# Optimization experiments

Measured on AMD Instinct MI355X. Metric: run time of the kernel, lower is better.

The kernel has to match this reference:

```python
import jax, jax.numpy as jnp
import numpy as np

NUM_SCOPES, NUM_DECOMPS, BATCH, NODES_IN, NUM_SUMS = 128, 8, 1024, 32, 32


def logmatmul(a, b):
    """Stable log-domain matmul: out[..., b, j] = logsumexp_k(a[..., b, k] + b[..., k, j]).
    a: [s, d, B, K], b: [s, d, K, J] -> [s, d, B, J]."""
    max_a = jnp.max(a, axis=-1, keepdims=True)            # [s, d, B, 1]
    max_b = jnp.max(b, axis=-2, keepdims=True)            # [s, d, 1, J]
    prod = jnp.einsum('sdbk,sdkj->sdbj', jnp.exp(a - max_a), jnp.exp(b - max_b))
    return jnp.log(prod) + max_a + max_b


def setup_inputs() -> dict:
    key = jax.random.key(0)
    k1, k2 = jax.random.split(key)
    x = jax.random.normal(k1, (NUM_SCOPES, NUM_DECOMPS, BATCH, NODES_IN), dtype=jnp.float32)
    # accumulators are linear-space (logspace_accumulators=False) and must be > 0
    accumulators = jax.random.uniform(
        k2, (NUM_SCOPES, NUM_DECOMPS, NODES_IN, NUM_SUMS),
        minval=0.1, maxval=1.0, dtype=jnp.float32)
    return {"x": x, "accumulators": accumulators}


def reference(x, accumulators):
    # log_softmax over the nodes_in axis (axis=2) of log(accumulators)
    log_weights = jax.nn.log_softmax(jnp.log(accumulators), axis=2)
    return logmatmul(x, log_weights)  # [s, d, B, num_sums]
```

## Files before the change

kernel.cpp:

```cpp
#include <hip/hip_runtime.h>
#include <stdint.h>


#define THREADS 256
#define ROWS    128

typedef __attribute__((ext_vector_type(8))) short short8;
typedef __attribute__((ext_vector_type(4))) float f32x4;
typedef __attribute__((ext_vector_type(4))) int   i32x4;

__device__ __forceinline__ uint32_t pack2_bf16(float lo, float hi) {
    uint32_t ul = __builtin_bit_cast(uint32_t, lo);
    uint32_t uh = __builtin_bit_cast(uint32_t, hi);
    ul = (ul + 0x7fffu + ((ul >> 16) & 1u)) >> 16;
    uh = (uh + 0x7fffu + ((uh >> 16) & 1u)) >> 16;
    return ul | (uh << 16);
}

__device__ __forceinline__ unsigned short bf16_1(float v) {
    uint32_t u = __builtin_bit_cast(uint32_t, v);
    return (unsigned short)((u + 0x7fffu + ((u >> 16) & 1u)) >> 16);
}

__global__ __launch_bounds__(THREADS, 8) void sws_kernel(
    const float* __restrict__ x,
    const float* __restrict__ acc,
    float* __restrict__ out)
{
    __shared__ float w_f32[32 * 32];
    __shared__ float inv_lds[32];
    __shared__ __align__(16) unsigned short wt_lds[32 * 32];

    const int t    = threadIdx.x;
    const int blk  = blockIdx.x;
    const int sd   = blk >> 3;
    const int lane = t & 63;
    const int wv   = t >> 6;
    const int l15  = lane & 15;
    const int quad = lane >> 4;

    const float4* x4 = (const float4*)(x + (size_t)blk * ROWS * 32);
    float4 xv[4];
#pragma unroll
    for (int i = 0; i < 2; ++i) {
        int f4 = ((wv * 2 + i) * 16 + l15) * 8 + quad * 2;
        xv[2 * i]     = x4[f4];
        xv[2 * i + 1] = x4[f4 + 1];
    }

    const float4 a4 = ((const float4*)(acc + (size_t)sd * 1024))[t];
    *((float4*)&w_f32[t * 4]) = a4;
    __syncthreads();
    if (t < 32) {
        float s = 0.f;
#pragma unroll
        for (int k = 0; k < 32; ++k) s += w_f32[k * 32 + t];
        inv_lds[t] = 1.0f / s;
    }
    __syncthreads();
    {
        const int k = t >> 3, j0 = (t & 7) * 4;
        const float4 inv4 = *((const float4*)&inv_lds[j0]);
        wt_lds[(j0 + 0) * 32 + k] = bf16_1(a4.x * inv4.x);
        wt_lds[(j0 + 1) * 32 + k] = bf16_1(a4.y * inv4.y);
        wt_lds[(j0 + 2) * 32 + k] = bf16_1(a4.z * inv4.z);
        wt_lds[(j0 + 3) * 32 + k] = bf16_1(a4.w * inv4.w);
    }

    float  mrow[2];
    short8 afrag[2];
#pragma unroll
    for (int i = 0; i < 2; ++i) {
        float4 a = xv[2 * i], b = xv[2 * i + 1];
        float m = fmaxf(fmaxf(fmaxf(a.x, a.y), fmaxf(a.z, a.w)),
                        fmaxf(fmaxf(b.x, b.y), fmaxf(b.z, b.w)));
        m = fmaxf(m, __shfl_xor(m, 16, 64));
        m = fmaxf(m, __shfl_xor(m, 32, 64));
        mrow[i] = m;
        i32x4 pk;
        pk[0] = (int)pack2_bf16(__expf(a.x - m), __expf(a.y - m));
        pk[1] = (int)pack2_bf16(__expf(a.z - m), __expf(a.w - m));
        pk[2] = (int)pack2_bf16(__expf(b.x - m), __expf(b.y - m));
        pk[3] = (int)pack2_bf16(__expf(b.z - m), __expf(b.w - m));
        afrag[i] = __builtin_bit_cast(short8, pk);
    }
    __syncthreads();

    short8 bfrag[2];
#pragma unroll
    for (int jt = 0; jt < 2; ++jt)
        bfrag[jt] = *(const short8*)&wt_lds[(jt * 16 + l15) * 32 + quad * 8];

    f32x4 cacc[2][2];
#pragma unroll
    for (int i = 0; i < 2; ++i)
#pragma unroll
        for (int jt = 0; jt < 2; ++jt)
            cacc[i][jt] = __builtin_amdgcn_mfma_f32_16x16x32_bf16(
                afrag[i], bfrag[jt], (f32x4){0.f, 0.f, 0.f, 0.f}, 0, 0, 0);

    float* ob = out + (size_t)blk * ROWS * 32;
#pragma unroll
    for (int i = 0; i < 2; ++i) {
        int rbase = ((wv * 2 + i) * 16) + quad * 4;
#pragma unroll
        for (int r = 0; r < 4; ++r) {
            float mr = __shfl(mrow[i], quad * 4 + r, 16);
            float* orow = ob + (size_t)(rbase + r) * 32;
            orow[l15]      = __logf(cacc[i][0][r]) + mr;
            orow[l15 + 16] = __logf(cacc[i][1][r]) + mr;
        }
    }
}

extern "C" void kernel_launch(void* const* d_in, const int* in_sizes, int n_in,
                              void* d_out, int out_size, void* d_ws, size_t ws_size,
                              hipStream_t stream) {
    const float* x   = (const float*)d_in[0];
    const float* acc = (const float*)d_in[1];
    float* out = (float*)d_out;

    dim3 grid(8192);
    dim3 block(THREADS);
    hipLaunchKernelGGL(sws_kernel, grid, block, 0, stream, x, acc, out);
}
```

Measured before the change: 231.1 us.

## Swap MFMA operands for float4 output stores and pad weight LDS pitch

The MFMA operands are swapped so each lane holds four consecutive output columns of a single row. Output can then be written as float4 stores, and the per-row max no longer needs a shuffle. The transposed weight tile in LDS gets a padded pitch of 40 to reduce bank conflicts on the scattered writes and fragment reads. The kernel is bandwidth-bound, so the main aim is fewer, wider global store instructions.

```diff
diff --git a/kernel.cpp b/kernel.cpp
--- a/kernel.cpp
+++ b/kernel.cpp
@@ -4,6 +4,7 @@
 
 #define THREADS 256
 #define ROWS    128
+#define WPITCH  40
 
 typedef __attribute__((ext_vector_type(8))) short short8;
 typedef __attribute__((ext_vector_type(4))) float f32x4;
@@ -29,7 +30,7 @@
 {
     __shared__ float w_f32[32 * 32];
     __shared__ float inv_lds[32];
-    __shared__ __align__(16) unsigned short wt_lds[32 * 32];
+    __shared__ __align__(16) unsigned short wt_lds[32 * WPITCH];
 
     const int t    = threadIdx.x;
     const int blk  = blockIdx.x;
@@ -61,10 +62,10 @@
     {
         const int k = t >> 3, j0 = (t & 7) * 4;
         const float4 inv4 = *((const float4*)&inv_lds[j0]);
-        wt_lds[(j0 + 0) * 32 + k] = bf16_1(a4.x * inv4.x);
-        wt_lds[(j0 + 1) * 32 + k] = bf16_1(a4.y * inv4.y);
-        wt_lds[(j0 + 2) * 32 + k] = bf16_1(a4.z * inv4.z);
-        wt_lds[(j0 + 3) * 32 + k] = bf16_1(a4.w * inv4.w);
+        wt_lds[(j0 + 0) * WPITCH + k] = bf16_1(a4.x * inv4.x);
+        wt_lds[(j0 + 1) * WPITCH + k] = bf16_1(a4.y * inv4.y);
+        wt_lds[(j0 + 2) * WPITCH + k] = bf16_1(a4.z * inv4.z);
+        wt_lds[(j0 + 3) * WPITCH + k] = bf16_1(a4.w * inv4.w);
     }
 
     float  mrow[2];
@@ -89,7 +90,7 @@
     short8 bfrag[2];
 #pragma unroll
     for (int jt = 0; jt < 2; ++jt)
-        bfrag[jt] = *(const short8*)&wt_lds[(jt * 16 + l15) * 32 + quad * 8];
+        bfrag[jt] = *(const short8*)&wt_lds[(jt * 16 + l15) * WPITCH + quad * 8];
 
     f32x4 cacc[2][2];
 #pragma unroll
@@ -97,18 +98,22 @@
 #pragma unroll
         for (int jt = 0; jt < 2; ++jt)
             cacc[i][jt] = __builtin_amdgcn_mfma_f32_16x16x32_bf16(
-                afrag[i], bfrag[jt], (f32x4){0.f, 0.f, 0.f, 0.f}, 0, 0, 0);
+                bfrag[jt], afrag[i], (f32x4){0.f, 0.f, 0.f, 0.f}, 0, 0, 0);
 
     float* ob = out + (size_t)blk * ROWS * 32;
 #pragma unroll
     for (int i = 0; i < 2; ++i) {
-        int rbase = ((wv * 2 + i) * 16) + quad * 4;
+        float* orow = ob + (size_t)((wv * 2 + i) * 16 + l15) * 32;
+        const float mr = mrow[i];
 #pragma unroll
-        for (int r = 0; r < 4; ++r) {
-            float mr = __shfl(mrow[i], quad * 4 + r, 16);
-            float* orow = ob + (size_t)(rbase + r) * 32;
-            orow[l15]      = __logf(cacc[i][0][r]) + mr;
-            orow[l15 + 16] = __logf(cacc[i][1][r]) + mr;
+        for (int jt = 0; jt < 2; ++jt) {
+            f32x4 c = cacc[i][jt];
+            float4 o;
+            o.x = __logf(c[0]) + mr;
+            o.y = __logf(c[1]) + mr;
+            o.z = __logf(c[2]) + mr;
+            o.w = __logf(c[3]) + mr;
+            *(float4*)(orow + jt * 16 + quad * 4) = o;
         }
     }
 }
```

After: 228.2 us. Within noise of the previous version (-1.3%).
